# Performance work log

Hardware: AMD Instinct MI355X
Metric: run time of the kernel (lower is better)

## Reference

```python
import jax, jax.numpy as jnp
import numpy as np

B, S, CIN, COUT, W, M, P = 32, 8192, 2, 1, 64, 16, 24


def setup_inputs() -> dict:
    key = jax.random.key(0)
    ks = jax.random.split(key, 12)

    def lin(k, o, i):
        return (jax.random.uniform(k, (o, i), jnp.float32) * 2 - 1) / np.float32(np.sqrt(i))

    scale = np.float32(1.0 / (W * W))  # SpectralConv1d init scale 1/(in*out)
    return {
        "x": jax.random.normal(ks[0], (B, S, CIN), jnp.float32),
        "fc0_w": lin(ks[1], W, CIN),
        "fc0_b": jnp.zeros((W,), jnp.float32),
        "conv_wr": jax.random.uniform(ks[2], (4, W, W, M), jnp.float32) * scale,
        "conv_wi": jax.random.uniform(ks[3], (4, W, W, M), jnp.float32) * scale,
        "pw_w": lin(ks[4], 4 * W, W).reshape(4, W, W),  # 1x1 conv weights (out,in)
        "pw_b": jnp.zeros((4, W), jnp.float32),
        "fc1_w": lin(ks[5], 128, W),
        "fc1_b": jnp.zeros((128,), jnp.float32),
        "fc2_w": lin(ks[6], COUT, 128),
        "ica_w": lin(ks[7], P, 128),
        "ica_b": jnp.zeros((P,), jnp.float32),
    }


def spectral_conv(h, wr, wi, n):
    # h: (B, W, S). Keep first M rfft modes, complex-multiply, inverse rfft.
    xf = jnp.fft.rfft(h, axis=-1)[..., :M]          # (B, W, M) complex
    w = wr + 1j * wi                                 # (W, W, M)
    of = jnp.einsum('bix,iox->box', xf, w)           # (B, W, M)
    of = jnp.pad(of, ((0, 0), (0, 0), (0, n // 2 + 1 - M)))
    return jnp.fft.irfft(of, n=n, axis=-1)


def reference(x, fc0_w, fc0_b, conv_wr, conv_wi, pw_w, pw_b, fc1_w, fc1_b, fc2_w, ica_w, ica_b):
    b, s, _ = x.shape
    h = x @ fc0_w.T + fc0_b                          # lift: (B, S, W)
    h = h.transpose(0, 2, 1)                         # (B, W, S)
    for l in range(4):
        x1 = spectral_conv(h, conv_wr[l], conv_wi[l], s)
        x2 = jnp.einsum('oi,bis->bos', pw_w[l], h) + pw_b[l][None, :, None]
        h = x1 + x2
        if l < 3:                                    # no relu after layer 3 (as in torch code)
            h = jax.nn.relu(h)
    h = h.transpose(0, 2, 1)                         # (B, S, W)
    h = h @ fc1_w.T + fc1_b                          # (B, S, 128)
    h_ = jax.nn.relu(h)
    # broadcast ICA decomposition: (B,S,1,128)*(1,1,COUT,128)
    components = h_[:, :, None, :] * fc2_w[None, None, :, :]
    tc = components @ ica_w.T + ica_b                # (B, S, COUT, P)
    out = tc.sum(-1)                                 # (B, S, COUT)
    return out, tc
```

## Files before the change

### kernel.cpp

```cpp
#include <hip/hip_runtime.h>
#include <math.h>

#define SB 8192
#define NB 32
#define WC 64
#define NM 16
#define NKC 32
#define NP 24
#define NSC 16
#define LP 132


__global__ __launch_bounds__(256) void k_table(float* __restrict__ T) {
    int s = blockIdx.x * 256 + threadIdx.x;
    float* row = T + (size_t)s * NKC;
    #pragma unroll
    for (int k = 0; k < NM; ++k) {
        int m = (k * s) & (SB - 1);
        double ang = (double)m * (6.283185307179586476925286766559 / (double)SB);
        row[2 * k]     = (float)cos(ang);
        row[2 * k + 1] = (float)sin(ang);
    }
}

__global__ __launch_bounds__(256) void k_prep(const float* __restrict__ ica_w,
                                              const float* __restrict__ fc2_w,
                                              float* __restrict__ icaT) {
    int tid = blockIdx.x * 256 + threadIdx.x;
    int c = tid / NP;
    int p = tid - c * NP;
    icaT[c * NP + p] = ica_w[p * 128 + c] * fc2_w[c];
}

__global__ __launch_bounds__(256) void k_prepw(const float* __restrict__ pw_w,
                                               float* __restrict__ pwT) {
    int tid = blockIdx.x * 256 + threadIdx.x;
    int l = tid >> 12, k = (tid >> 6) & 63, o = tid & 63;
    pwT[tid] = pw_w[(size_t)l * 4096 + o * 64 + k];
}

__global__ __launch_bounds__(256) void k_lift(const float* __restrict__ x,
                                              const float* __restrict__ fc0_w,
                                              const float* __restrict__ fc0_b,
                                              float* __restrict__ h) {
    int b = blockIdx.y;
    int s = blockIdx.x * 256 + threadIdx.x;
    float2 xv = ((const float2*)x)[(size_t)b * SB + s];
    #pragma unroll
    for (int w = 0; w < WC; ++w) {
        float v = fmaf(xv.x, fc0_w[2 * w], fmaf(xv.y, fc0_w[2 * w + 1], fc0_b[w]));
        h[((size_t)(b * WC + w)) * SB + s] = v;
    }
}

__global__ __launch_bounds__(256) void k_dft(const float* __restrict__ h,
                                             const float* __restrict__ T,
                                             float* __restrict__ xfp) {
    __shared__ float hT[64][LP];
    __shared__ float Tt[32][LP];
    int blk = blockIdx.x;
    int b  = blk >> 4;
    int sc = blk & (NSC - 1);
    int t  = threadIdx.x;
    int g = t >> 4, j = t & 15;

    float acc[4][2];
    #pragma unroll
    for (int i = 0; i < 4; ++i) { acc[i][0] = 0.f; acc[i][1] = 0.f; }

    const float* hb = h + (size_t)b * WC * SB;
    int ch   = t >> 2;
    int part = t & 3;
    int sl   = t >> 1;
    int jj0  = (t & 1) * 16;

    for (int st = 0; st < 4; ++st) {
        int s_base = sc * 512 + st * 128;

        const float* hrow = hb + (size_t)ch * SB + s_base;
        #pragma unroll
        for (int r = 0; r < 8; ++r) {
            int so = (part + 4 * r) * 4;
            *(float4*)&hT[ch][so] = *(const float4*)(hrow + so);
        }
        {
            const float4* src = (const float4*)(T + (size_t)(s_base + sl) * NKC + jj0);
            float4 a = src[0], c4 = src[1], d = src[2], e = src[3];
            Tt[jj0 +  0][sl] = a.x;  Tt[jj0 +  1][sl] = a.y;
            Tt[jj0 +  2][sl] = a.z;  Tt[jj0 +  3][sl] = a.w;
            Tt[jj0 +  4][sl] = c4.x; Tt[jj0 +  5][sl] = c4.y;
            Tt[jj0 +  6][sl] = c4.z; Tt[jj0 +  7][sl] = c4.w;
            Tt[jj0 +  8][sl] = d.x;  Tt[jj0 +  9][sl] = d.y;
            Tt[jj0 + 10][sl] = d.z;  Tt[jj0 + 11][sl] = d.w;
            Tt[jj0 + 12][sl] = e.x;  Tt[jj0 + 13][sl] = e.y;
            Tt[jj0 + 14][sl] = e.z;  Tt[jj0 + 15][sl] = e.w;
        }
        __syncthreads();

        #pragma unroll 4
        for (int step = 0; step < 32; ++step) {
            int s4 = step * 4;
            float4 ta = *(const float4*)&Tt[j][s4];
            float4 tb = *(const float4*)&Tt[j + 16][s4];
            #pragma unroll
            for (int i = 0; i < 4; ++i) {
                float4 hv = *(const float4*)&hT[g * 4 + i][s4];
                acc[i][0] = fmaf(hv.x, ta.x, fmaf(hv.y, ta.y,
                            fmaf(hv.z, ta.z, fmaf(hv.w, ta.w, acc[i][0]))));
                acc[i][1] = fmaf(hv.x, tb.x, fmaf(hv.y, tb.y,
                            fmaf(hv.z, tb.z, fmaf(hv.w, tb.w, acc[i][1]))));
            }
        }
        __syncthreads();
    }

    float* dst = xfp + ((size_t)(sc * NB + b)) * 2048;
    #pragma unroll
    for (int i = 0; i < 4; ++i) {
        dst[(g * 4 + i) * 32 + j]      = acc[i][0];
        dst[(g * 4 + i) * 32 + j + 16] = acc[i][1];
    }
}

__global__ __launch_bounds__(256) void k_red(const float* __restrict__ xfp,
                                             float* __restrict__ xf) {
    int idx = blockIdx.x * 256 + threadIdx.x;
    int b = idx >> 11;
    int r = idx & 2047;
    float s = 0.f;
    #pragma unroll
    for (int sc = 0; sc < NSC; ++sc)
        s += xfp[((size_t)(sc * NB + b)) * 2048 + r];
    xf[idx] = s;
}

__global__ __launch_bounds__(256) void k_mix(const float* __restrict__ xf,
                                             const float* __restrict__ wr,
                                             const float* __restrict__ wi,
                                             float* __restrict__ ofT) {
    int tid = blockIdx.x * 256 + threadIdx.x;
    int k = tid & 15;
    int o = (tid >> 4) & 63;
    int b = tid >> 10;
    float orr = 0.f, oii = 0.f;
    const float2* xfb = (const float2*)(xf + (size_t)b * WC * NKC);
    #pragma unroll 4
    for (int i = 0; i < WC; ++i) {
        float2 cs = xfb[i * NM + k];
        float wrv = wr[(i * WC + o) * NM + k];
        float wiv = wi[(i * WC + o) * NM + k];
        orr = fmaf(cs.x, wrv, fmaf(cs.y, wiv, orr));
        oii = fmaf(cs.x, wiv, fmaf(-cs.y, wrv, oii));
    }
    float alpha = (k == 0 ? 1.f : 2.f) / (float)SB;
    ofT[((size_t)b * NKC + 2 * k) * 64 + o]     = alpha * orr;
    ofT[((size_t)b * NKC + 2 * k + 1) * 64 + o] = -alpha * oii;
}

__global__ __launch_bounds__(256) void k_update(float* __restrict__ h,
                                                const float* __restrict__ T,
                                                const float* __restrict__ ofT,
                                                const float* __restrict__ pwT,
                                                const float* __restrict__ pwb,
                                                int relu) {
    __shared__ float hS[96][LP];
    int t = threadIdx.x;
    int b = blockIdx.y;
    int s0 = blockIdx.x * 128;
    int lane_s = t & 63;
    int g = __builtin_amdgcn_readfirstlane((t >> 6) & 3);
    int ob = g * 16;

    {
        int ch = t >> 2, part = t & 3;
        const float* hrow = h + ((size_t)(b * WC + ch)) * SB + s0;
        #pragma unroll
        for (int r = 0; r < 8; ++r) {
            int so = (part + 4 * r) * 4;
            *(float4*)&hS[ch][so] = *(const float4*)(hrow + so);
        }
    }
    {
        int sl = t >> 1, jj0 = (t & 1) * 16;
        const float4* src = (const float4*)(T + (size_t)(s0 + sl) * NKC + jj0);
        float4 a = src[0], c4 = src[1], d = src[2], e = src[3];
        hS[64 + jj0 +  0][sl] = a.x;  hS[64 + jj0 +  1][sl] = a.y;
        hS[64 + jj0 +  2][sl] = a.z;  hS[64 + jj0 +  3][sl] = a.w;
        hS[64 + jj0 +  4][sl] = c4.x; hS[64 + jj0 +  5][sl] = c4.y;
        hS[64 + jj0 +  6][sl] = c4.z; hS[64 + jj0 +  7][sl] = c4.w;
        hS[64 + jj0 +  8][sl] = d.x;  hS[64 + jj0 +  9][sl] = d.y;
        hS[64 + jj0 + 10][sl] = d.z;  hS[64 + jj0 + 11][sl] = d.w;
        hS[64 + jj0 + 12][sl] = e.x;  hS[64 + jj0 + 13][sl] = e.y;
        hS[64 + jj0 + 14][sl] = e.z;  hS[64 + jj0 + 15][sl] = e.w;
    }
    __syncthreads();

    float acc0[16], acc1[16];
    #pragma unroll
    for (int o = 0; o < 16; ++o) { acc0[o] = pwb[ob + o]; acc1[o] = pwb[ob + o]; }

    const float* wbase0 = pwT + ob;
    const float* wbase1 = ofT + ((size_t)b * NKC) * 64 + ob;

    for (int kc = 0; kc < 8; ++kc) {
        #pragma unroll
        for (int u = 0; u < 8; ++u) {
            int k = kc * 8 + u;
            float h0 = hS[k][lane_s];
            float h1 = hS[k][64 + lane_s];
            const float* w = wbase0 + k * 64;
            #pragma unroll
            for (int o = 0; o < 16; ++o) {
                acc0[o] = fmaf(w[o], h0, acc0[o]);
                acc1[o] = fmaf(w[o], h1, acc1[o]);
            }
        }
    }
    for (int kc = 0; kc < 4; ++kc) {
        #pragma unroll
        for (int u = 0; u < 8; ++u) {
            int j = kc * 8 + u;
            float h0 = hS[64 + j][lane_s];
            float h1 = hS[64 + j][64 + lane_s];
            const float* w = wbase1 + j * 64;
            #pragma unroll
            for (int o = 0; o < 16; ++o) {
                acc0[o] = fmaf(w[o], h0, acc0[o]);
                acc1[o] = fmaf(w[o], h1, acc1[o]);
            }
        }
    }

    float* hw0 = h + (size_t)b * WC * SB + s0 + lane_s;
    float* hw1 = hw0 + 64;
    #pragma unroll
    for (int o = 0; o < 16; ++o) {
        float v0 = acc0[o], v1 = acc1[o];
        if (relu) { v0 = fmaxf(v0, 0.f); v1 = fmaxf(v1, 0.f); }
        hw0[(size_t)(ob + o) * SB] = v0;
        hw1[(size_t)(ob + o) * SB] = v1;
    }
}

__global__ __launch_bounds__(256) void k_final(const float* __restrict__ h,
                                               const float* __restrict__ fc1_w,
                                               const float* __restrict__ fc1_b,
                                               const float* __restrict__ icaT,
                                               const float* __restrict__ ica_b,
                                               float* __restrict__ out,
                                               float* __restrict__ tc) {
    __shared__ float u_lds[6400];
    float (*hS)[68] = (float(*)[68])u_lds;
    int t = threadIdx.x;
    int b = blockIdx.y;
    int s0 = blockIdx.x * 64;
    int lane_s = t & 63;
    int wv = __builtin_amdgcn_readfirstlane(t >> 6);
    int c0 = wv * 32;

    {
        int sl = t & 63, chg = t >> 6;
        const float* hb = h + (size_t)b * WC * SB + s0 + sl;
        #pragma unroll
        for (int cc = 0; cc < 16; ++cc) {
            int ch = chg * 16 + cc;
            hS[sl][ch] = hb[(size_t)ch * SB];
        }
    }
    __syncthreads();

    float acc[NP];
    #pragma unroll
    for (int p = 0; p < NP; ++p) acc[p] = 0.f;

    for (int cq = 0; cq < 8; ++cq) {
        int c = c0 + 4 * cq;
        float tv0 = fc1_b[c], tv1 = fc1_b[c + 1], tv2 = fc1_b[c + 2], tv3 = fc1_b[c + 3];
        const float* w0 = fc1_w + (size_t)c * WC;
        const float* w1 = w0 + WC;
        const float* w2 = w1 + WC;
        const float* w3 = w2 + WC;
        for (int ioct = 0; ioct < 8; ++ioct) {
            float4 xa = *(const float4*)&hS[lane_s][ioct * 8];
            float4 xb = *(const float4*)&hS[lane_s][ioct * 8 + 4];
            float xs[8] = {xa.x, xa.y, xa.z, xa.w, xb.x, xb.y, xb.z, xb.w};
            #pragma unroll
            for (int u = 0; u < 8; ++u) {
                int i = ioct * 8 + u;
                tv0 = fmaf(w0[i], xs[u], tv0);
                tv1 = fmaf(w1[i], xs[u], tv1);
                tv2 = fmaf(w2[i], xs[u], tv2);
                tv3 = fmaf(w3[i], xs[u], tv3);
            }
        }
        tv0 = fmaxf(tv0, 0.f); tv1 = fmaxf(tv1, 0.f);
        tv2 = fmaxf(tv2, 0.f); tv3 = fmaxf(tv3, 0.f);
        const float* e0 = icaT + (size_t)c * NP;
        const float* e1 = e0 + NP;
        const float* e2 = e1 + NP;
        const float* e3 = e2 + NP;
        #pragma unroll
        for (int p = 0; p < NP; ++p)
            acc[p] = fmaf(tv0, e0[p], fmaf(tv1, e1[p],
                     fmaf(tv2, e2[p], fmaf(tv3, e3[p], acc[p]))));
    }

    __syncthreads();
    {
        float* slot = u_lds + ((t >> 6) * 64 + lane_s) * 25;
        #pragma unroll
        for (int p = 0; p < NP; ++p) slot[p] = acc[p];
    }
    __syncthreads();

    float* tcb = tc + ((size_t)b * SB + s0) * NP;
    #pragma unroll
    for (int r = 0; r < 6; ++r) {
        int e = t + r * 256;
        int s = e / NP, p = e - s * NP;
        float v = u_lds[s * 25 + p] + u_lds[(64 + s) * 25 + p]
                + u_lds[(128 + s) * 25 + p] + u_lds[(192 + s) * 25 + p]
                + ica_b[p];
        tcb[e] = v;
        u_lds[s * 25 + p] = v;
    }
    __syncthreads();
    if (t < 64) {
        float osum = 0.f;
        #pragma unroll
        for (int p = 0; p < NP; ++p) osum += u_lds[t * 25 + p];
        out[(size_t)b * SB + s0 + t] = osum;
    }
}

extern "C" void kernel_launch(void* const* d_in, const int* in_sizes, int n_in,
                              void* d_out, int out_size, void* d_ws, size_t ws_size,
                              hipStream_t stream) {
    const float* x     = (const float*)d_in[0];
    const float* fc0_w = (const float*)d_in[1];
    const float* fc0_b = (const float*)d_in[2];
    const float* cwr   = (const float*)d_in[3];
    const float* cwi   = (const float*)d_in[4];
    const float* pw_w  = (const float*)d_in[5];
    const float* pw_b  = (const float*)d_in[6];
    const float* fc1_w = (const float*)d_in[7];
    const float* fc1_b = (const float*)d_in[8];
    const float* fc2_w = (const float*)d_in[9];
    const float* ica_w = (const float*)d_in[10];
    const float* ica_b = (const float*)d_in[11];

    float* out = (float*)d_out;
    float* tc  = out + (size_t)NB * SB;

    float* ws   = (float*)d_ws;
    float* h    = ws;
    float* T    = ws + 16777216;
    float* xf   = ws + 17039360;
    float* ofT  = ws + 17104896;
    float* icaT = ws + 17170432;
    float* pwT  = ws + 17173504;
    float* xfp  = tc;

    k_table<<<32, 256, 0, stream>>>(T);
    k_prep<<<12, 256, 0, stream>>>(ica_w, fc2_w, icaT);
    k_prepw<<<64, 256, 0, stream>>>(pw_w, pwT);
    k_lift<<<dim3(32, 32), 256, 0, stream>>>(x, fc0_w, fc0_b, h);

    for (int l = 0; l < 4; ++l) {
        k_dft<<<NB * NSC, 256, 0, stream>>>(h, T, xfp);
        k_red<<<256, 256, 0, stream>>>(xfp, xf);
        k_mix<<<128, 256, 0, stream>>>(xf, cwr + (size_t)l * WC * WC * NM,
                                       cwi + (size_t)l * WC * WC * NM, ofT);
        k_update<<<dim3(64, 32), 256, 0, stream>>>(h, T, ofT,
                                                   pwT + (size_t)l * 4096,
                                                   pw_b + (size_t)l * WC,
                                                   (l < 3) ? 1 : 0);
    }

    k_final<<<dim3(128, 32), 256, 0, stream>>>(h, fc1_w, fc1_b, icaT, ica_b, out, tc);
}
```

Baseline: 443.8 us.

## Restructure forward DFT kernel with per-wave sample split and larger register tiles

The forward DFT kernel now has each wavefront handle a quarter of the 128-sample chunk. Every thread accumulates an 8-channel by 4-mode register tile, replacing the previous 4x2 tile, which raises FMA-to-LDS-load reuse. The h tile is stored transposed (sample-major) in shared memory, and the twiddle table is copied directly without a transpose. The four waves' partial sums are then reduced through shared memory and written as coalesced float4 stores. This adds a cross-wave reduction pass, more accumulator registers, and scattered scalar LDS writes during the transpose, which may cause bank conflicts.

```diff
diff --git a/kernel.cpp b/kernel.cpp
--- a/kernel.cpp
+++ b/kernel.cpp
@@ -56,70 +56,89 @@
 __global__ __launch_bounds__(256) void k_dft(const float* __restrict__ h,
                                              const float* __restrict__ T,
                                              float* __restrict__ xfp) {
-    __shared__ float hT[64][LP];
-    __shared__ float Tt[32][LP];
+    __shared__ float u[12800];
     int blk = blockIdx.x;
     int b  = blk >> 4;
     int sc = blk & (NSC - 1);
     int t  = threadIdx.x;
-    int g = t >> 4, j = t & 15;
-
-    float acc[4][2];
-    #pragma unroll
-    for (int i = 0; i < 4; ++i) { acc[i][0] = 0.f; acc[i][1] = 0.f; }
-
-    const float* hb = h + (size_t)b * WC * SB;
-    int ch   = t >> 2;
-    int part = t & 3;
-    int sl   = t >> 1;
-    int jj0  = (t & 1) * 16;
+    int lane = t & 63;
+    int wv = __builtin_amdgcn_readfirstlane(t >> 6);
+    int g  = lane >> 3;
+    int j8 = lane & 7;
+
+    float acc[8][4];
+    #pragma unroll
+    for (int i = 0; i < 8; ++i)
+        #pragma unroll
+        for (int m = 0; m < 4; ++m) acc[i][m] = 0.f;
+
+    int ch_s = t >> 2, part = t & 3;
+    const float* hb = h + ((size_t)(b * WC + ch_s)) * SB;
 
     for (int st = 0; st < 4; ++st) {
         int s_base = sc * 512 + st * 128;
 
-        const float* hrow = hb + (size_t)ch * SB + s_base;
+        const float* hrow = hb + s_base;
         #pragma unroll
         for (int r = 0; r < 8; ++r) {
             int so = (part + 4 * r) * 4;
-            *(float4*)&hT[ch][so] = *(const float4*)(hrow + so);
+            float4 v = *(const float4*)(hrow + so);
+            u[(so + 0) * 68 + ch_s] = v.x;
+            u[(so + 1) * 68 + ch_s] = v.y;
+            u[(so + 2) * 68 + ch_s] = v.z;
+            u[(so + 3) * 68 + ch_s] = v.w;
         }
         {
-            const float4* src = (const float4*)(T + (size_t)(s_base + sl) * NKC + jj0);
-            float4 a = src[0], c4 = src[1], d = src[2], e = src[3];
-            Tt[jj0 +  0][sl] = a.x;  Tt[jj0 +  1][sl] = a.y;
-            Tt[jj0 +  2][sl] = a.z;  Tt[jj0 +  3][sl] = a.w;
-            Tt[jj0 +  4][sl] = c4.x; Tt[jj0 +  5][sl] = c4.y;
-            Tt[jj0 +  6][sl] = c4.z; Tt[jj0 +  7][sl] = c4.w;
-            Tt[jj0 +  8][sl] = d.x;  Tt[jj0 +  9][sl] = d.y;
-            Tt[jj0 + 10][sl] = d.z;  Tt[jj0 + 11][sl] = d.w;
-            Tt[jj0 + 12][sl] = e.x;  Tt[jj0 + 13][sl] = e.y;
-            Tt[jj0 + 14][sl] = e.z;  Tt[jj0 + 15][sl] = e.w;
+            const float4* tsrc = (const float4*)(T + (size_t)s_base * NKC);
+            float4* tdst = (float4*)(u + 8704);
+            #pragma unroll
+            for (int r = 0; r < 4; ++r) tdst[t + r * 256] = tsrc[t + r * 256];
         }
         __syncthreads();
 
         #pragma unroll 4
-        for (int step = 0; step < 32; ++step) {
-            int s4 = step * 4;
-            float4 ta = *(const float4*)&Tt[j][s4];
-            float4 tb = *(const float4*)&Tt[j + 16][s4];
-            #pragma unroll
-            for (int i = 0; i < 4; ++i) {
-                float4 hv = *(const float4*)&hT[g * 4 + i][s4];
-                acc[i][0] = fmaf(hv.x, ta.x, fmaf(hv.y, ta.y,
-                            fmaf(hv.z, ta.z, fmaf(hv.w, ta.w, acc[i][0]))));
-                acc[i][1] = fmaf(hv.x, tb.x, fmaf(hv.y, tb.y,
-                            fmaf(hv.z, tb.z, fmaf(hv.w, tb.w, acc[i][1]))));
+        for (int ss = 0; ss < 32; ++ss) {
+            int s = wv * 32 + ss;
+            float4 tv = *(const float4*)&u[8704 + s * 32 + j8 * 4];
+            float4 h0 = *(const float4*)&u[s * 68 + g * 8];
+            float4 h1 = *(const float4*)&u[s * 68 + g * 8 + 4];
+            float hh[8] = {h0.x, h0.y, h0.z, h0.w, h1.x, h1.y, h1.z, h1.w};
+            #pragma unroll
+            for (int i = 0; i < 8; ++i) {
+                acc[i][0] = fmaf(hh[i], tv.x, acc[i][0]);
+                acc[i][1] = fmaf(hh[i], tv.y, acc[i][1]);
+                acc[i][2] = fmaf(hh[i], tv.z, acc[i][2]);
+                acc[i][3] = fmaf(hh[i], tv.w, acc[i][3]);
             }
         }
         __syncthreads();
     }
 
+    {
+        float* slot = u + (wv * 64 + lane) * 33;
+        #pragma unroll
+        for (int i = 0; i < 8; ++i)
+            #pragma unroll
+            for (int m = 0; m < 4; ++m) slot[i * 4 + m] = acc[i][m];
+    }
+    __syncthreads();
+
     float* dst = xfp + ((size_t)(sc * NB + b)) * 2048;
-    #pragma unroll
-    for (int i = 0; i < 4; ++i) {
-        dst[(g * 4 + i) * 32 + j]      = acc[i][0];
-        dst[(g * 4 + i) * 32 + j + 16] = acc[i][1];
-    }
+    float res[8];
+    #pragma unroll
+    for (int e = 0; e < 8; ++e) {
+        int idx = t * 8 + e;
+        int ch = idx >> 5, mode = idx & 31;
+        int g2 = ch >> 3, i2 = ch & 7;
+        int q2 = mode >> 2, m2 = mode & 3;
+        int lane2 = g2 * 8 + q2;
+        int v2 = i2 * 4 + m2;
+        res[e] = u[lane2 * 33 + v2] + u[(64 + lane2) * 33 + v2]
+               + u[(128 + lane2) * 33 + v2] + u[(192 + lane2) * 33 + v2];
+    }
+    float4* d4 = (float4*)(dst + t * 8);
+    d4[0] = make_float4(res[0], res[1], res[2], res[3]);
+    d4[1] = make_float4(res[4], res[5], res[6], res[7]);
 }
 
 __global__ __launch_bounds__(256) void k_red(const float* __restrict__ xfp,
```

After: 434.8 us. 2.0% less time.
